# Performance work log

Measured on AMD Instinct MI355X. Metric: run time of the kernel, lower is better.

The kernel has to match this reference:

```python
import jax, jax.numpy as jnp
import numpy as np

N_NODES = 50000
N_EDGES = 250000
D_NODE = 128
D_EMB = 200
D_STATIC = 64
F = 2 * D_NODE + D_EMB + D_STATIC  # 520
D_OUT = 8


def setup_inputs() -> dict:
    key = jax.random.key(0)
    ks = jax.random.split(key, 10)
    X = jax.random.normal(ks[0], (N_NODES, D_NODE), dtype=jnp.float32)
    edge_index = jax.random.randint(ks[1], (2, N_EDGES), 0, N_NODES, dtype=jnp.int64)
    edge_embedding = jax.random.normal(ks[2], (N_EDGES, D_EMB), dtype=jnp.float32)
    static_edge_features = jax.random.normal(ks[3], (N_EDGES, D_STATIC), dtype=jnp.float32)
    s = 1.0 / np.sqrt(F)
    W1 = jax.random.normal(ks[4], (F, F), dtype=jnp.float32) * s
    b1 = jax.random.normal(ks[5], (F,), dtype=jnp.float32) * s
    W2 = jax.random.normal(ks[6], (F, F), dtype=jnp.float32) * s
    b2 = jax.random.normal(ks[7], (F,), dtype=jnp.float32) * s
    Wout = jax.random.normal(ks[8], (F, D_OUT), dtype=jnp.float32) * s
    bout = jax.random.normal(ks[9], (D_OUT,), dtype=jnp.float32) * s
    return {"X": X, "edge_index": edge_index, "edge_embedding": edge_embedding,
            "static_edge_features": static_edge_features,
            "W1": W1, "b1": b1, "W2": W2, "b2": b2, "Wout": Wout, "bout": bout}


def reference(X, edge_index, edge_embedding, static_edge_features, W1, b1, W2, b2, Wout, bout):
    src, dst = edge_index[0], edge_index[1]
    # gather paired node features + edge embedding + static features -> [E, F]
    h = jnp.concatenate([X[src], X[dst], edge_embedding, static_edge_features], axis=-1)
    # dense layers: ELU(Linear) with residual connections (dropout = 0, eval mode)
    for W, b in ((W1, b1), (W2, b2)):
        h = jax.nn.elu(h @ W + b) + h
    return h @ Wout + bout
```

## Files before the change

kernel.cpp:

```cpp
#include <hip/hip_runtime.h>
#include <hip/hip_bf16.h>

#define E_EDGES   250000
#define D_NODE    128
#define D_EMB     200
#define D_STATIC  64
#define F_DIM     520
#define NT        33
#define KT        17
#define RS        552
#define BM        64
#define SMEM_BYTES (BM * RS * 2)

typedef __attribute__((ext_vector_type(8))) short frag_t;
typedef __attribute__((ext_vector_type(4))) float f32x4;

__device__ __forceinline__ unsigned int cvtpk(float lo, float hi) {
    unsigned int r;
    asm("v_cvt_pk_bf16_f32 %0, %1, %2" : "=v"(r) : "v"(lo), "v"(hi));
    return r;
}

__device__ __forceinline__ unsigned short f2bf(float x) {
    union { float f; unsigned int u; } v; v.f = x;
    unsigned int r = v.u + 0x7FFFu + ((v.u >> 16) & 1u);
    return (unsigned short)(r >> 16);
}
__device__ __forceinline__ float bf2f(unsigned short u) {
    union { float f; unsigned int i; } v; v.i = ((unsigned int)u) << 16; return v.f;
}
__device__ __forceinline__ float elu(float z) {
    return (z > 0.0f) ? z : (__expf(z) - 1.0f);
}

__global__ void pack_w_kernel(const float* __restrict__ W, unsigned short* __restrict__ Wp,
                              int ntiles, int krows, int ncols, int ldw) {
    int t = blockIdx.x * blockDim.x + threadIdx.x;
    if (t >= ntiles * KT * 64) return;
    int nt   = t / (KT * 64);
    int rem  = t % (KT * 64);
    int kt   = rem / 64;
    int lane = rem % 64;
    int n  = nt * 16 + (lane & 15);
    int kb = kt * 32 + (lane >> 4) * 8;
    unsigned short v[8];
    #pragma unroll
    for (int j = 0; j < 8; ++j) {
        int k = kb + j;
        float w = (k < krows && n < ncols) ? W[(long long)k * ldw + n] : 0.0f;
        v[j] = f2bf(w);
    }
    unsigned short* dst = Wp + (long long)t * 8;
    #pragma unroll
    for (int j = 0; j < 8; ++j) dst[j] = v[j];
}

__device__ __forceinline__ void layer_pass(char* __restrict__ h,
                                           const unsigned short* __restrict__ Wp,
                                           const float* __restrict__ bias,
                                           int wave, int lane) {
    const int idx = lane & 15;
    const int grp = lane >> 4;
    const int nt0 = wave * 4;
    const bool t32 = (wave < 4);
    const char* wb = (const char*)Wp + (size_t)lane * 16;
    const char* abase   = h + (size_t)idx * (RS * 2) + grp * 16;
    const char* a32base = h + (size_t)(wave * 16 + idx) * (RS * 2) + grp * 16;

    f32x4 acc[4][4];
    #pragma unroll
    for (int t = 0; t < 4; ++t)
        #pragma unroll
        for (int m = 0; m < 4; ++m)
            acc[t][m] = (f32x4){0.f, 0.f, 0.f, 0.f};
    f32x4 acc32 = (f32x4){0.f, 0.f, 0.f, 0.f};

    #pragma unroll 1
    for (int kt = 0; kt < KT; ++kt) {
        frag_t b[4];
        #pragma unroll
        for (int t = 0; t < 4; ++t)
            b[t] = *(const frag_t*)(wb + (size_t)((nt0 + t) * KT + kt) * 1024);
        frag_t b32, a32;
        if (t32) {
            b32 = *(const frag_t*)(wb + (size_t)(32 * KT + kt) * 1024);
            a32 = *(const frag_t*)(a32base + kt * 64);
        }
        {
            frag_t a[2];
            #pragma unroll
            for (int m = 0; m < 2; ++m)
                a[m] = *(const frag_t*)(abase + (size_t)(m * 16) * (RS * 2) + kt * 64);
            #pragma unroll
            for (int t = 0; t < 4; ++t)
                #pragma unroll
                for (int m = 0; m < 2; ++m)
                    acc[t][m] = __builtin_amdgcn_mfma_f32_16x16x32_bf16(b[t], a[m], acc[t][m], 0, 0, 0);
        }
        {
            frag_t a[2];
            #pragma unroll
            for (int m = 0; m < 2; ++m)
                a[m] = *(const frag_t*)(abase + (size_t)((m + 2) * 16) * (RS * 2) + kt * 64);
            #pragma unroll
            for (int t = 0; t < 4; ++t)
                #pragma unroll
                for (int m = 0; m < 2; ++m)
                    acc[t][m + 2] = __builtin_amdgcn_mfma_f32_16x16x32_bf16(b[t], a[m], acc[t][m + 2], 0, 0, 0);
        }
        if (t32)
            acc32 = __builtin_amdgcn_mfma_f32_16x16x32_bf16(b32, a32, acc32, 0, 0, 0);
    }

    __syncthreads();

    #pragma unroll
    for (int t = 0; t < 4; ++t) {
        const int colb = (nt0 + t) * 16 + grp * 4;
        const float4 bb = *(const float4*)(bias + colb);
        #pragma unroll
        for (int m = 0; m < 4; ++m) {
            const int row = m * 16 + idx;
            char* p = h + (size_t)row * (RS * 2) + (size_t)colb * 2;
            ushort4 hv = *(const ushort4*)p;
            float z0 = elu(acc[t][m][0] + bb.x) + bf2f(hv.x);
            float z1 = elu(acc[t][m][1] + bb.y) + bf2f(hv.y);
            float z2 = elu(acc[t][m][2] + bb.z) + bf2f(hv.z);
            float z3 = elu(acc[t][m][3] + bb.w) + bf2f(hv.w);
            *(uint2*)p = make_uint2(cvtpk(z0, z1), cvtpk(z2, z3));
        }
    }
    if (t32) {
        const int colb = 512 + grp * 4;
        float bb[4];
        #pragma unroll
        for (int q = 0; q < 4; ++q) bb[q] = (colb + q < F_DIM) ? bias[colb + q] : 0.0f;
        const int row = wave * 16 + idx;
        char* p = h + (size_t)row * (RS * 2) + (size_t)colb * 2;
        ushort4 hv = *(const ushort4*)p;
        float z0 = elu(acc32[0] + bb[0]) + bf2f(hv.x);
        float z1 = elu(acc32[1] + bb[1]) + bf2f(hv.y);
        float z2 = elu(acc32[2] + bb[2]) + bf2f(hv.z);
        float z3 = elu(acc32[3] + bb[3]) + bf2f(hv.w);
        *(uint2*)p = make_uint2(cvtpk(z0, z1), cvtpk(z2, z3));
    }
    __syncthreads();
}

__global__ __launch_bounds__(512, 4)
void edge_mlp_kernel(const float* __restrict__ X, const int* __restrict__ eidx,
                     const float* __restrict__ emb, const float* __restrict__ sef,
                     const float* __restrict__ b1, const float* __restrict__ b2,
                     const float* __restrict__ bout,
                     const unsigned short* __restrict__ W1p,
                     const unsigned short* __restrict__ W2p,
                     const unsigned short* __restrict__ Woutp,
                     float* __restrict__ out) {
    extern __shared__ char h[];
    const int tid  = threadIdx.x;
    const int wave = tid >> 6;
    const int lane = tid & 63;
    const long long base = (long long)blockIdx.x * BM;

    int myidx = 0;
    if (lane < 16) {
        long long e = base + wave * 8 + (lane & 7);
        if (e >= E_EDGES) e = E_EDGES - 1;
        myidx = eidx[(long long)(lane >> 3) * E_EDGES + e];
    }

    #pragma unroll 1
    for (int g = 0; g < 2; ++g) {
        #pragma unroll
        for (int rr = 0; rr < 4; ++rr) {
            const int r = wave * 8 + g * 4 + rr;
            char* row = h + (size_t)r * (RS * 2);
            const int src = __shfl(myidx, g * 4 + rr);
            const int dst = __shfl(myidx, 8 + g * 4 + rr);
            float2 v = *(const float2*)(X + (long long)src * D_NODE + lane * 2);
            *(unsigned int*)(row + lane * 4) = cvtpk(v.x, v.y);
            float2 w = *(const float2*)(X + (long long)dst * D_NODE + lane * 2);
            *(unsigned int*)(row + 256 + lane * 4) = cvtpk(w.x, w.y);
        }
    }
    #pragma unroll 1
    for (int g = 0; g < 2; ++g) {
        #pragma unroll
        for (int rr = 0; rr < 4; ++rr) {
            if (lane < 50) {
                long long e = base + wave * 8 + g * 4 + rr;
                if (e >= E_EDGES) e = E_EDGES - 1;
                char* row = h + (size_t)(wave * 8 + g * 4 + rr) * (RS * 2);
                float4 v = *(const float4*)(emb + e * D_EMB + (long long)lane * 4);
                *(uint2*)(row + 512 + lane * 8) =
                    make_uint2(cvtpk(v.x, v.y), cvtpk(v.z, v.w));
            }
        }
    }
    #pragma unroll 1
    for (int q = 0; q < 2; ++q) {
        const int r = wave * 8 + q * 4 + (lane >> 4);
        long long e = base + r;
        if (e >= E_EDGES) e = E_EDGES - 1;
        char* row = h + (size_t)r * (RS * 2);
        float4 v = *(const float4*)(sef + e * D_STATIC + (long long)(lane & 15) * 4);
        *(uint2*)(row + 912 + (lane & 15) * 8) =
            make_uint2(cvtpk(v.x, v.y), cvtpk(v.z, v.w));
        if ((lane & 15) < 6)
            *(uint2*)(row + 1040 + (lane & 15) * 8) = make_uint2(0u, 0u);
    }
    __syncthreads();

    layer_pass(h, W1p, b1, wave, lane);
    layer_pass(h, W2p, b2, wave, lane);

    if (wave < 4) {
        const int idx = lane & 15;
        const int grp = lane >> 4;
        f32x4 acc = (f32x4){0.f, 0.f, 0.f, 0.f};
        #pragma unroll 1
        for (int kt = 0; kt < KT; ++kt) {
            frag_t b = *(const frag_t*)((const char*)Woutp + (size_t)kt * 1024 + (size_t)lane * 16);
            frag_t a = *(const frag_t*)(h + (size_t)(wave * 16 + idx) * (RS * 2) + kt * 64 + grp * 16);
            acc = __builtin_amdgcn_mfma_f32_16x16x32_bf16(b, a, acc, 0, 0, 0);
        }
        if (grp < 2) {
            const long long e = base + wave * 16 + idx;
            if (e < E_EDGES) {
                float4 bb = *(const float4*)(bout + grp * 4);
                float4 o = make_float4(acc[0] + bb.x, acc[1] + bb.y,
                                       acc[2] + bb.z, acc[3] + bb.w);
                *(float4*)(out + e * 8 + grp * 4) = o;
            }
        }
    }
}

extern "C" void kernel_launch(void* const* d_in, const int* in_sizes, int n_in,
                              void* d_out, int out_size, void* d_ws, size_t ws_size,
                              hipStream_t stream) {
    const float* X    = (const float*)d_in[0];
    const int*   eidx = (const int*)d_in[1];
    const float* emb  = (const float*)d_in[2];
    const float* sef  = (const float*)d_in[3];
    const float* W1   = (const float*)d_in[4];
    const float* b1   = (const float*)d_in[5];
    const float* W2   = (const float*)d_in[6];
    const float* b2   = (const float*)d_in[7];
    const float* Wout = (const float*)d_in[8];
    const float* bout = (const float*)d_in[9];
    float* out = (float*)d_out;

    unsigned short* W1p   = (unsigned short*)d_ws;
    unsigned short* W2p   = W1p + (size_t)NT * KT * 512;
    unsigned short* Woutp = W2p + (size_t)NT * KT * 512;

    int total = NT * KT * 64;
    pack_w_kernel<<<(total + 255) / 256, 256, 0, stream>>>(W1, W1p, NT, F_DIM, F_DIM, F_DIM);
    pack_w_kernel<<<(total + 255) / 256, 256, 0, stream>>>(W2, W2p, NT, F_DIM, F_DIM, F_DIM);
    pack_w_kernel<<<(KT * 64 + 255) / 256, 256, 0, stream>>>(Wout, Woutp, 1, F_DIM, 8, 8);

    (void)hipFuncSetAttribute((const void*)edge_mlp_kernel,
                              hipFuncAttributeMaxDynamicSharedMemorySize, SMEM_BYTES);
    int nblocks = (E_EDGES + BM - 1) / BM;
    edge_mlp_kernel<<<nblocks, 512, SMEM_BYTES, stream>>>(
        X, eidx, emb, sef, b1, b2, bout, W1p, W2p, Woutp, out);
}
```

Measured before the change: 350.9 us.

## Switch hidden-layer GEMMs to 32x32x16 MFMA tiles with double-buffered weight loads

Replaces the 16x16x32 MFMA tiling of the two 520x520 layers with 32x32x16 MFMAs. Each wave now computes two 32-column tiles across two 32-row halves, and the leftover 8 columns are handled by a separate 16x16 path. Weights are repacked into a new 32-wide fragment layout and biases are padded so they can be read as aligned float4. Weight fragment loads are double-buffered across k-steps. The aim is fewer MFMA issues and fewer LDS A-loads per FLOP, at the cost of more accumulator registers under launch bounds of 512 threads with 4 blocks per CU.

```diff
diff --git a/kernel.cpp b/kernel.cpp
--- a/kernel.cpp
+++ b/kernel.cpp
@@ -6,21 +6,22 @@
 #define D_EMB     200
 #define D_STATIC  64
 #define F_DIM     520
-#define NT        33
+#define CT32      16
+#define KT32      34
 #define KT        17
 #define RS        552
 #define BM        64
 #define SMEM_BYTES (BM * RS * 2)
 
-typedef __attribute__((ext_vector_type(8))) short frag_t;
-typedef __attribute__((ext_vector_type(4))) float f32x4;
+typedef __attribute__((ext_vector_type(8)))  short frag_t;
+typedef __attribute__((ext_vector_type(4)))  float f32x4;
+typedef __attribute__((ext_vector_type(16))) float f32x16;
 
 __device__ __forceinline__ unsigned int cvtpk(float lo, float hi) {
     unsigned int r;
     asm("v_cvt_pk_bf16_f32 %0, %1, %2" : "=v"(r) : "v"(lo), "v"(hi));
     return r;
 }
-
 __device__ __forceinline__ unsigned short f2bf(float x) {
     union { float f; unsigned int u; } v; v.f = x;
     unsigned int r = v.u + 0x7FFFu + ((v.u >> 16) & 1u);
@@ -31,6 +32,27 @@
 }
 __device__ __forceinline__ float elu(float z) {
     return (z > 0.0f) ? z : (__expf(z) - 1.0f);
+}
+
+__global__ void pack_w32_kernel(const float* __restrict__ W, unsigned short* __restrict__ Wq,
+                                int ldw) {
+    int t = blockIdx.x * blockDim.x + threadIdx.x;
+    if (t >= CT32 * KT32 * 64) return;
+    int ct   = t / (KT32 * 64);
+    int rem  = t % (KT32 * 64);
+    int kt   = rem / 64;
+    int lane = rem % 64;
+    int n  = ct * 32 + (lane & 31);
+    int kb = kt * 16 + (lane >> 5) * 8;
+    unsigned short v[8];
+    #pragma unroll
+    for (int j = 0; j < 8; ++j) {
+        int k = kb + j;
+        v[j] = (k < F_DIM) ? f2bf(W[(long long)k * ldw + n]) : (unsigned short)0;
+    }
+    unsigned short* dst = Wq + (long long)t * 8;
+    #pragma unroll
+    for (int j = 0; j < 8; ++j) dst[j] = v[j];
 }
 
 __global__ void pack_w_kernel(const float* __restrict__ W, unsigned short* __restrict__ Wp,
@@ -55,93 +77,92 @@
     for (int j = 0; j < 8; ++j) dst[j] = v[j];
 }
 
+__global__ void pack_bias_kernel(const float* __restrict__ b, float* __restrict__ bp) {
+    int i = blockIdx.x * blockDim.x + threadIdx.x;
+    if (i < 544) bp[i] = (i < F_DIM) ? b[i] : 0.0f;
+}
+
 __device__ __forceinline__ void layer_pass(char* __restrict__ h,
-                                           const unsigned short* __restrict__ Wp,
-                                           const float* __restrict__ bias,
+                                           const unsigned short* __restrict__ Wq,
+                                           const unsigned short* __restrict__ Wr,
+                                           const float* __restrict__ biasp,
                                            int wave, int lane) {
+    const int l31 = lane & 31;
+    const int hi  = lane >> 5;
     const int idx = lane & 15;
     const int grp = lane >> 4;
-    const int nt0 = wave * 4;
+    const int ct0 = wave * 2;
     const bool t32 = (wave < 4);
-    const char* wb = (const char*)Wp + (size_t)lane * 16;
-    const char* abase   = h + (size_t)idx * (RS * 2) + grp * 16;
+    const char* wb  = (const char*)Wq + (size_t)lane * 16;
+    const char* wbr = (const char*)Wr + (size_t)lane * 16;
+    const char* abase   = h + (size_t)l31 * (RS * 2) + hi * 16;
     const char* a32base = h + (size_t)(wave * 16 + idx) * (RS * 2) + grp * 16;
 
-    f32x4 acc[4][4];
-    #pragma unroll
-    for (int t = 0; t < 4; ++t)
+    f32x16 acc00 = {0}, acc01 = {0}, acc10 = {0}, acc11 = {0};
+    f32x4  accr  = (f32x4){0.f, 0.f, 0.f, 0.f};
+
+    auto loadB = [&](frag_t* d, int kt) {
+        d[0] = *(const frag_t*)(wb + (size_t)((ct0 + 0) * KT32 + kt) * 1024);
+        d[1] = *(const frag_t*)(wb + (size_t)((ct0 + 1) * KT32 + kt) * 1024);
+    };
+    auto step = [&](const frag_t* b, int kt) {
+        frag_t a0 = *(const frag_t*)(abase + kt * 32);
+        frag_t a1 = *(const frag_t*)(abase + (size_t)32 * (RS * 2) + kt * 32);
+        if (t32 && (kt & 1) == 0) {
+            frag_t b32 = *(const frag_t*)(wbr + (size_t)(kt >> 1) * 1024);
+            frag_t a32 = *(const frag_t*)(a32base + (kt >> 1) * 64);
+            accr = __builtin_amdgcn_mfma_f32_16x16x32_bf16(b32, a32, accr, 0, 0, 0);
+        }
+        acc00 = __builtin_amdgcn_mfma_f32_32x32x16_bf16(b[0], a0, acc00, 0, 0, 0);
+        acc01 = __builtin_amdgcn_mfma_f32_32x32x16_bf16(b[0], a1, acc01, 0, 0, 0);
+        acc10 = __builtin_amdgcn_mfma_f32_32x32x16_bf16(b[1], a0, acc10, 0, 0, 0);
+        acc11 = __builtin_amdgcn_mfma_f32_32x32x16_bf16(b[1], a1, acc11, 0, 0, 0);
+    };
+
+    frag_t bA[2], bB[2];
+    loadB(bA, 0);
+    #pragma unroll 1
+    for (int kp = 0; kp < 17; ++kp) {
+        loadB(bB, 2 * kp + 1);
+        step(bA, 2 * kp);
+        if (kp < 16) loadB(bA, 2 * kp + 2);
+        step(bB, 2 * kp + 1);
+    }
+
+    __syncthreads();
+
+    #pragma unroll
+    for (int ct = 0; ct < 2; ++ct) {
         #pragma unroll
-        for (int m = 0; m < 4; ++m)
-            acc[t][m] = (f32x4){0.f, 0.f, 0.f, 0.f};
-    f32x4 acc32 = (f32x4){0.f, 0.f, 0.f, 0.f};
-
-    #pragma unroll 1
-    for (int kt = 0; kt < KT; ++kt) {
-        frag_t b[4];
-        #pragma unroll
-        for (int t = 0; t < 4; ++t)
-            b[t] = *(const frag_t*)(wb + (size_t)((nt0 + t) * KT + kt) * 1024);
-        frag_t b32, a32;
-        if (t32) {
-            b32 = *(const frag_t*)(wb + (size_t)(32 * KT + kt) * 1024);
-            a32 = *(const frag_t*)(a32base + kt * 64);
-        }
-        {
-            frag_t a[2];
+        for (int rt = 0; rt < 2; ++rt) {
+            const f32x16 a = (ct == 0) ? (rt == 0 ? acc00 : acc01)
+                                       : (rt == 0 ? acc10 : acc11);
+            const int row = rt * 32 + l31;
+            char* prow = h + (size_t)row * (RS * 2);
             #pragma unroll
-            for (int m = 0; m < 2; ++m)
-                a[m] = *(const frag_t*)(abase + (size_t)(m * 16) * (RS * 2) + kt * 64);
-            #pragma unroll
-            for (int t = 0; t < 4; ++t)
-                #pragma unroll
-                for (int m = 0; m < 2; ++m)
-                    acc[t][m] = __builtin_amdgcn_mfma_f32_16x16x32_bf16(b[t], a[m], acc[t][m], 0, 0, 0);
-        }
-        {
-            frag_t a[2];
-            #pragma unroll
-            for (int m = 0; m < 2; ++m)
-                a[m] = *(const frag_t*)(abase + (size_t)((m + 2) * 16) * (RS * 2) + kt * 64);
-            #pragma unroll
-            for (int t = 0; t < 4; ++t)
-                #pragma unroll
-                for (int m = 0; m < 2; ++m)
-                    acc[t][m + 2] = __builtin_amdgcn_mfma_f32_16x16x32_bf16(b[t], a[m], acc[t][m + 2], 0, 0, 0);
-        }
-        if (t32)
-            acc32 = __builtin_amdgcn_mfma_f32_16x16x32_bf16(b32, a32, acc32, 0, 0, 0);
-    }
-
-    __syncthreads();
-
-    #pragma unroll
-    for (int t = 0; t < 4; ++t) {
-        const int colb = (nt0 + t) * 16 + grp * 4;
-        const float4 bb = *(const float4*)(bias + colb);
-        #pragma unroll
-        for (int m = 0; m < 4; ++m) {
-            const int row = m * 16 + idx;
-            char* p = h + (size_t)row * (RS * 2) + (size_t)colb * 2;
-            ushort4 hv = *(const ushort4*)p;
-            float z0 = elu(acc[t][m][0] + bb.x) + bf2f(hv.x);
-            float z1 = elu(acc[t][m][1] + bb.y) + bf2f(hv.y);
-            float z2 = elu(acc[t][m][2] + bb.z) + bf2f(hv.z);
-            float z3 = elu(acc[t][m][3] + bb.w) + bf2f(hv.w);
-            *(uint2*)p = make_uint2(cvtpk(z0, z1), cvtpk(z2, z3));
+            for (int g = 0; g < 4; ++g) {
+                const int n0 = (ct0 + ct) * 32 + g * 8 + hi * 4;
+                const float4 bb = *(const float4*)(biasp + n0);
+                char* p = prow + (size_t)n0 * 2;
+                ushort4 hv = *(const ushort4*)p;
+                float z0 = elu(a[g * 4 + 0] + bb.x) + bf2f(hv.x);
+                float z1 = elu(a[g * 4 + 1] + bb.y) + bf2f(hv.y);
+                float z2 = elu(a[g * 4 + 2] + bb.z) + bf2f(hv.z);
+                float z3 = elu(a[g * 4 + 3] + bb.w) + bf2f(hv.w);
+                *(uint2*)p = make_uint2(cvtpk(z0, z1), cvtpk(z2, z3));
+            }
         }
     }
     if (t32) {
         const int colb = 512 + grp * 4;
-        float bb[4];
-        #pragma unroll
-        for (int q = 0; q < 4; ++q) bb[q] = (colb + q < F_DIM) ? bias[colb + q] : 0.0f;
+        const float4 bb = *(const float4*)(biasp + colb);
         const int row = wave * 16 + idx;
         char* p = h + (size_t)row * (RS * 2) + (size_t)colb * 2;
         ushort4 hv = *(const ushort4*)p;
-        float z0 = elu(acc32[0] + bb[0]) + bf2f(hv.x);
-        float z1 = elu(acc32[1] + bb[1]) + bf2f(hv.y);
-        float z2 = elu(acc32[2] + bb[2]) + bf2f(hv.z);
-        float z3 = elu(acc32[3] + bb[3]) + bf2f(hv.w);
+        float z0 = elu(accr[0] + bb.x) + bf2f(hv.x);
+        float z1 = elu(accr[1] + bb.y) + bf2f(hv.y);
+        float z2 = elu(accr[2] + bb.z) + bf2f(hv.z);
+        float z3 = elu(accr[3] + bb.w) + bf2f(hv.w);
         *(uint2*)p = make_uint2(cvtpk(z0, z1), cvtpk(z2, z3));
     }
     __syncthreads();
@@ -150,10 +171,12 @@
 __global__ __launch_bounds__(512, 4)
 void edge_mlp_kernel(const float* __restrict__ X, const int* __restrict__ eidx,
                      const float* __restrict__ emb, const float* __restrict__ sef,
-                     const float* __restrict__ b1, const float* __restrict__ b2,
                      const float* __restrict__ bout,
-                     const unsigned short* __restrict__ W1p,
-                     const unsigned short* __restrict__ W2p,
+                     const float* __restrict__ b1p, const float* __restrict__ b2p,
+                     const unsigned short* __restrict__ W1q,
+                     const unsigned short* __restrict__ W2q,
+                     const unsigned short* __restrict__ W1r,
+                     const unsigned short* __restrict__ W2r,
                      const unsigned short* __restrict__ Woutp,
                      float* __restrict__ out) {
     extern __shared__ char h[];
@@ -192,8 +215,7 @@
                 if (e >= E_EDGES) e = E_EDGES - 1;
                 char* row = h + (size_t)(wave * 8 + g * 4 + rr) * (RS * 2);
                 float4 v = *(const float4*)(emb + e * D_EMB + (long long)lane * 4);
-                *(uint2*)(row + 512 + lane * 8) =
-                    make_uint2(cvtpk(v.x, v.y), cvtpk(v.z, v.w));
+                *(uint2*)(row + 512 + lane * 8) = make_uint2(cvtpk(v.x, v.y), cvtpk(v.z, v.w));
             }
         }
     }
@@ -204,15 +226,14 @@
         if (e >= E_EDGES) e = E_EDGES - 1;
         char* row = h + (size_t)r * (RS * 2);
         float4 v = *(const float4*)(sef + e * D_STATIC + (long long)(lane & 15) * 4);
-        *(uint2*)(row + 912 + (lane & 15) * 8) =
-            make_uint2(cvtpk(v.x, v.y), cvtpk(v.z, v.w));
+        *(uint2*)(row + 912 + (lane & 15) * 8) = make_uint2(cvtpk(v.x, v.y), cvtpk(v.z, v.w));
         if ((lane & 15) < 6)
             *(uint2*)(row + 1040 + (lane & 15) * 8) = make_uint2(0u, 0u);
     }
     __syncthreads();
 
-    layer_pass(h, W1p, b1, wave, lane);
-    layer_pass(h, W2p, b2, wave, lane);
+    layer_pass(h, W1q, W1r, b1p, wave, lane);
+    layer_pass(h, W2q, W2r, b2p, wave, lane);
 
     if (wave < 4) {
         const int idx = lane & 15;
@@ -228,9 +249,8 @@
             const long long e = base + wave * 16 + idx;
             if (e < E_EDGES) {
                 float4 bb = *(const float4*)(bout + grp * 4);
-                float4 o = make_float4(acc[0] + bb.x, acc[1] + bb.y,
-                                       acc[2] + bb.z, acc[3] + bb.w);
-                *(float4*)(out + e * 8 + grp * 4) = o;
+                *(float4*)(out + e * 8 + grp * 4) =
+                    make_float4(acc[0] + bb.x, acc[1] + bb.y, acc[2] + bb.z, acc[3] + bb.w);
             }
         }
     }
@@ -251,18 +271,28 @@
     const float* bout = (const float*)d_in[9];
     float* out = (float*)d_out;
 
-    unsigned short* W1p   = (unsigned short*)d_ws;
-    unsigned short* W2p   = W1p + (size_t)NT * KT * 512;
-    unsigned short* Woutp = W2p + (size_t)NT * KT * 512;
-
-    int total = NT * KT * 64;
-    pack_w_kernel<<<(total + 255) / 256, 256, 0, stream>>>(W1, W1p, NT, F_DIM, F_DIM, F_DIM);
-    pack_w_kernel<<<(total + 255) / 256, 256, 0, stream>>>(W2, W2p, NT, F_DIM, F_DIM, F_DIM);
+    const size_t W32SZ = (size_t)CT32 * KT32 * 512;
+    const size_t W16SZ = (size_t)KT * 512;
+    unsigned short* W1q   = (unsigned short*)d_ws;
+    unsigned short* W2q   = W1q + W32SZ;
+    unsigned short* W1r   = W2q + W32SZ;
+    unsigned short* W2r   = W1r + W16SZ;
+    unsigned short* Woutp = W2r + W16SZ;
+    float* b1p = (float*)(Woutp + W16SZ);
+    float* b2p = b1p + 544;
+
+    int t32tot = CT32 * KT32 * 64;
+    pack_w32_kernel<<<(t32tot + 255) / 256, 256, 0, stream>>>(W1, W1q, F_DIM);
+    pack_w32_kernel<<<(t32tot + 255) / 256, 256, 0, stream>>>(W2, W2q, F_DIM);
+    pack_w_kernel<<<(KT * 64 + 255) / 256, 256, 0, stream>>>(W1 + 512, W1r, 1, F_DIM, 8, F_DIM);
+    pack_w_kernel<<<(KT * 64 + 255) / 256, 256, 0, stream>>>(W2 + 512, W2r, 1, F_DIM, 8, F_DIM);
     pack_w_kernel<<<(KT * 64 + 255) / 256, 256, 0, stream>>>(Wout, Woutp, 1, F_DIM, 8, 8);
+    pack_bias_kernel<<<3, 256, 0, stream>>>(b1, b1p);
+    pack_bias_kernel<<<3, 256, 0, stream>>>(b2, b2p);
 
     (void)hipFuncSetAttribute((const void*)edge_mlp_kernel,
                               hipFuncAttributeMaxDynamicSharedMemorySize, SMEM_BYTES);
     int nblocks = (E_EDGES + BM - 1) / BM;
     edge_mlp_kernel<<<nblocks, 512, SMEM_BYTES, stream>>>(
-        X, eidx, emb, sef, b1, b2, bout, W1p, W2p, Woutp, out);
-}
+        X, eidx, emb, sef, bout, b1p, b2p, W1q, W2q, W1r, W2r, Woutp, out);
+}
```

Result: slower. 408.0 us (+16.3%).
